# Optimization experiments

Hardware: AMD Instinct MI355X
Metric: run time of the kernel (lower is better)

Reference implementation:

```python
import jax, jax.numpy as jnp
import numpy as np

N = 50000
E = 1600000
NFEAT = 256
NHID = 256
PAD_N = 60000


def setup_inputs() -> dict:
    key = jax.random.key(0)
    ks = jax.random.split(key, 8)
    x = jax.random.normal(ks[0], (N, NFEAT), dtype=jnp.float32)
    adj_rows = jax.random.randint(ks[1], (E,), 0, N)
    adj_cols = jax.random.randint(ks[2], (E,), 0, N)
    adj_vals = jax.random.uniform(ks[3], (E,), dtype=jnp.float32)
    pos_idx = jnp.arange(N)  # unique rows within padded output
    W1 = jax.random.normal(ks[4], (NFEAT, NHID), dtype=jnp.float32) * 0.05
    b1 = jax.random.normal(ks[5], (NHID,), dtype=jnp.float32) * 0.05
    W2 = jax.random.normal(ks[6], (NHID, NHID), dtype=jnp.float32) * 0.05
    b2 = jax.random.normal(ks[7], (NHID,), dtype=jnp.float32) * 0.05
    return {"x": x, "adj_rows": adj_rows, "adj_cols": adj_cols,
            "adj_vals": adj_vals, "pad_n": PAD_N, "pos_idx": pos_idx,
            "W1": W1, "b1": b1, "W2": W2, "b2": b2}


def _graph_conv(x, rows, cols, vals, W, b):
    # support = x @ W ; out = adj @ support + b  (adj in COO form)
    support = x @ W                                   # [N, H]
    msgs = vals[:, None] * support[cols]              # [E, H] gather + scale
    agg = jax.ops.segment_sum(msgs, rows, num_segments=x.shape[0])
    return agg + b


def reference(x, adj_rows, adj_cols, adj_vals, pad_n, pos_idx, W1, b1, W2, b2):
    h = jax.nn.relu(_graph_conv(x, adj_rows, adj_cols, adj_vals, W1, b1))
    # dropout: eval mode (training=False) -> identity
    h = jax.nn.relu(_graph_conv(h, adj_rows, adj_cols, adj_vals, W2, b2))
    out = jnp.zeros((pad_n, h.shape[1]), dtype=h.dtype)
    out = out.at[pos_idx].set(h)
    return out
```

## Files before the change

kernel.cpp:

```cpp
#include <hip/hip_runtime.h>
#include <hip/hip_bf16.h>

typedef __attribute__((ext_vector_type(8))) short short8;
typedef __attribute__((ext_vector_type(4))) float f32x4;
typedef __attribute__((ext_vector_type(2))) float f32x2;

#define BUK_SHIFT 7
#define BUK_ROWS 128
#define MAXBUK 400
#define CAP2 6144
#define CHUNK 6250
#define CHUNK_PAD 6272

static __device__ __forceinline__ unsigned short f2bf(float f) {
    unsigned u = __float_as_uint(f);
    u += 0x7fffu + ((u >> 16) & 1u);
    return (unsigned short)(u >> 16);
}
static __device__ __forceinline__ unsigned pk2bf(float a, float b) {
    return (unsigned)f2bf(a) | ((unsigned)f2bf(b) << 16);
}

__global__ void wtr_kernel(const float* __restrict__ W1, const float* __restrict__ W2,
                           unsigned short* __restrict__ W1t, unsigned short* __restrict__ W2t) {
    int k = blockIdx.x, n = threadIdx.x;
    const float* W = blockIdx.y ? W2 : W1;
    unsigned short* Wt = blockIdx.y ? W2t : W1t;
    Wt[n * 256 + k] = f2bf(W[k * 256 + n]);
}


__global__ __launch_bounds__(1024) void bin_count(const int* __restrict__ rows,
                                                  int* __restrict__ cntM, int E, int nbuk) {
    __shared__ int c[MAXBUK];
    for (int i = threadIdx.x; i < nbuk; i += 1024) c[i] = 0;
    __syncthreads();
    int s = blockIdx.x * CHUNK, e = s + CHUNK < E ? s + CHUNK : E;
    for (int i = s + (int)threadIdx.x; i < e; i += 1024) atomicAdd(&c[rows[i] >> BUK_SHIFT], 1);
    __syncthreads();
    for (int i = threadIdx.x; i < nbuk; i += 1024) cntM[i * gridDim.x + blockIdx.x] = c[i];
}

__global__ __launch_bounds__(1024) void scan1_kernel(const int* __restrict__ in,
                                                     int* __restrict__ tmp,
                                                     int* __restrict__ bsum, int n) {
    __shared__ int sdata[1024];
    int i = blockIdx.x * 1024 + threadIdx.x;
    int v = (i < n) ? in[i] : 0;
    sdata[threadIdx.x] = v;
    __syncthreads();
    for (int off = 1; off < 1024; off <<= 1) {
        int t = (threadIdx.x >= (unsigned)off) ? sdata[threadIdx.x - off] : 0;
        __syncthreads();
        sdata[threadIdx.x] += t;
        __syncthreads();
    }
    if (i < n) tmp[i] = sdata[threadIdx.x] - v;
    if (threadIdx.x == 1023) bsum[blockIdx.x] = sdata[1023];
}

__global__ __launch_bounds__(512) void scan2_kernel(const int* __restrict__ bsum,
                                                    int* __restrict__ boff, int nb) {
    __shared__ int s[512];
    int t = threadIdx.x;
    int v = (t < nb) ? bsum[t] : 0;
    s[t] = v;
    __syncthreads();
    for (int off = 1; off < 512; off <<= 1) {
        int x = (t >= off) ? s[t - off] : 0;
        __syncthreads();
        s[t] += x;
        __syncthreads();
    }
    if (t < nb) boff[t] = s[t] - v;
}

static __device__ __forceinline__ int scanv(const int* __restrict__ tmp,
                                            const int* __restrict__ boff, int idx) {
    return tmp[idx] + boff[idx >> 10];
}

__global__ __launch_bounds__(1024) void bin_scatter(const int* __restrict__ rows,
                                                    const int* __restrict__ cols,
                                                    const float* __restrict__ vals,
                                                    const int* __restrict__ tmp,
                                                    const int* __restrict__ boff,
                                                    unsigned int* __restrict__ cc,
                                                    unsigned char* __restrict__ rb,
                                                    int E, int nbuk, int nblk) {
    __shared__ unsigned int scc[CHUNK_PAD];
    __shared__ unsigned char srb[CHUNK_PAD];
    __shared__ int lcnt[512], lsc[512], lcur[512];
    const int b = blockIdx.x, tid = threadIdx.x;
    const int s = b * CHUNK, e = s + CHUNK < E ? s + CHUNK : E;
    if (tid < 512) lcnt[tid] = 0;
    __syncthreads();
    for (int i = s + tid; i < e; i += 1024) atomicAdd(&lcnt[rows[i] >> BUK_SHIFT], 1);
    __syncthreads();
    if (tid < 512) lsc[tid] = lcnt[tid];
    __syncthreads();
    for (int off = 1; off < 512; off <<= 1) {
        int t = (tid < 512 && tid >= off) ? lsc[tid - off] : 0;
        __syncthreads();
        if (tid < 512) lsc[tid] += t;
        __syncthreads();
    }
    if (tid < 512) lcur[tid] = lsc[tid] - lcnt[tid];
    __syncthreads();
    for (int i = s + tid; i < e; i += 1024) {
        int r = rows[i];
        int p = atomicAdd(&lcur[r >> BUK_SHIFT], 1);
        scc[p] = ((unsigned)cols[i] << 16) | (unsigned)f2bf(vals[i]);
        srb[p] = (unsigned char)(r & (BUK_ROWS - 1));
    }
    __syncthreads();
    const int wv = tid >> 6, ln = tid & 63;
    for (int bu = wv; bu < nbuk; bu += 16) {
        const int lo = lsc[bu] - lcnt[bu];
        const int n = lcnt[bu];
        const int gbase = scanv(tmp, boff, bu * nblk + b);
        for (int j = ln; j < n; j += 64) {
            cc[gbase + j] = scc[lo + j];
            rb[gbase + j] = srb[lo + j];
        }
    }
}

__global__ __launch_bounds__(1024) void bucket_pad(const unsigned int* __restrict__ cc,
                                                   const unsigned char* __restrict__ rb,
                                                   const int* __restrict__ tmp,
                                                   const int* __restrict__ boff,
                                                   unsigned int* __restrict__ cc2,
                                                   int2* __restrict__ rp,
                                                   int E, int nbuk, int nblk, int N) {
    __shared__ int cnt[BUK_ROWS];
    __shared__ int psc[BUK_ROWS];
    __shared__ int cur[BUK_ROWS];
    const int b = blockIdx.x;
    const int tid = threadIdx.x;
    const int base = scanv(tmp, boff, b * nblk);
    const int end = (b + 1 < nbuk) ? scanv(tmp, boff, (b + 1) * nblk) : E;
    const int sz = end - base;
    if (tid < BUK_ROWS) cnt[tid] = 0;
    __syncthreads();
    for (int i = tid; i < sz; i += 1024) atomicAdd(&cnt[rb[base + i]], 1);
    __syncthreads();
    if (tid < BUK_ROWS) psc[tid] = (cnt[tid] + 7) & ~7;
    __syncthreads();
    for (int off = 1; off < BUK_ROWS; off <<= 1) {
        int t = (tid < BUK_ROWS && tid >= off) ? psc[tid - off] : 0;
        __syncthreads();
        if (tid < BUK_ROWS) psc[tid] += t;
        __syncthreads();
    }
    if (tid < BUK_ROWS) {
        int c = cnt[tid];
        int pc = (c + 7) & ~7;
        int excl = psc[tid] - pc;
        cur[tid] = excl;
        int st = b * CAP2 + excl;
        rp[b * BUK_ROWS + tid] = make_int2(st, st + pc);
        for (int z = c; z < pc; ++z) cc2[(size_t)st + z] = 0u;
    }
    __syncthreads();
    for (int i = tid; i < sz; i += 1024) {
        int p = atomicAdd(&cur[rb[base + i]], 1);
        cc2[(size_t)b * CAP2 + p] = cc[base + i];
    }
}

template <int AF32>
static __device__ __forceinline__ uint4 load_frag(const char* p) {
    if (AF32) {
        const float* f = (const float*)p;
        float4 f0 = *reinterpret_cast<const float4*>(f);
        float4 f1 = *reinterpret_cast<const float4*>(f + 4);
        uint4 u;
        u.x = pk2bf(f0.x, f0.y); u.y = pk2bf(f0.z, f0.w);
        u.z = pk2bf(f1.x, f1.y); u.w = pk2bf(f1.z, f1.w);
        return u;
    }
    return *reinterpret_cast<const uint4*>(p);
}

template <int AF32>
__global__ __launch_bounds__(256) void gemm_kernel(const void* __restrict__ Av,
                                                   const unsigned short* __restrict__ Bt,
                                                   unsigned char* __restrict__ S8, int M) {
    __shared__ unsigned char lds[2][8192];
    const int esz = AF32 ? 4 : 2;
    const int tid = threadIdx.x;
    const int lane = tid & 63;
    const int wave = tid >> 6;
    const int m0 = blockIdx.x * 64;
    const int l15 = lane & 15;
    const int q = lane >> 4;
    const int sw = (l15 & 7) << 4;

    const int st_r0 = tid >> 3;
    const int st_c = tid & 7;
    const int st_off0 = st_r0 * 128 + ((st_c ^ (st_r0 & 7)) << 4);
    const int st_r1 = st_r0 + 32;
    const int st_off1 = st_r1 * 128 + ((st_c ^ (st_r1 & 7)) << 4);
    int row0 = m0 + st_r0; row0 = row0 < M ? row0 : 0;
    int row1 = m0 + st_r1; row1 = row1 < M ? row1 : 0;
    const char* s0p = (const char*)Av + ((size_t)row0 * 256 + st_c * 8) * esz;
    const char* s1p = (const char*)Av + ((size_t)row1 * 256 + st_c * 8) * esz;

    const unsigned short* bb = Bt + (size_t)(wave * 64 + l15) * 256 + q * 8;

    f32x4 acc[4][4] = {};

    uint4 s0 = load_frag<AF32>(s0p);
    uint4 s1 = load_frag<AF32>(s1p);
    *reinterpret_cast<uint4*>(&lds[0][st_off0]) = s0;
    *reinterpret_cast<uint4*>(&lds[0][st_off1]) = s1;
    __syncthreads();

#pragma unroll
    for (int it = 0; it < 4; ++it) {
        const int buf = it & 1;
        if (it < 3) {
            s0 = load_frag<AF32>(s0p + (size_t)(it + 1) * 64 * esz);
            s1 = load_frag<AF32>(s1p + (size_t)(it + 1) * 64 * esz);
        }
        const int kk = it * 64;
#pragma unroll
        for (int ks = 0; ks < 2; ++ks) {
            short8 a[4], b[4];
#pragma unroll
            for (int mf = 0; mf < 4; ++mf) {
                int r = mf * 16 + l15;
                a[mf] = *reinterpret_cast<const short8*>(
                    &lds[buf][r * 128 + ((ks * 64 + q * 16) ^ sw)]);
            }
#pragma unroll
            for (int nf = 0; nf < 4; ++nf)
                b[nf] = *reinterpret_cast<const short8*>(bb + (size_t)nf * 16 * 256 + kk + ks * 32);
#pragma unroll
            for (int mf = 0; mf < 4; ++mf)
#pragma unroll
                for (int nf = 0; nf < 4; ++nf)
                    acc[mf][nf] = __builtin_amdgcn_mfma_f32_16x16x32_bf16(b[nf], a[mf], acc[mf][nf], 0, 0, 0);
        }
        if (it < 3) {
            *reinterpret_cast<uint4*>(&lds[buf ^ 1][st_off0]) = s0;
            *reinterpret_cast<uint4*>(&lds[buf ^ 1][st_off1]) = s1;
        }
        __syncthreads();
    }

    const int g4 = q * 4;
#pragma unroll
    for (int mf = 0; mf < 4; ++mf) {
        int m = m0 + mf * 16 + l15;
        if (m < M) {
#pragma unroll
            for (int nf = 0; nf < 4; ++nf) {
                int p = __builtin_amdgcn_cvt_pk_fp8_f32(acc[mf][nf][0], acc[mf][nf][1], 0, false);
                p = __builtin_amdgcn_cvt_pk_fp8_f32(acc[mf][nf][2], acc[mf][nf][3], p, true);
                *reinterpret_cast<int*>(S8 + ((size_t)wave * M + m) * 64 + nf * 16 + g4) = p;
            }
        }
    }
}

template <int LAYER2>
__global__ __launch_bounds__(256) void spmm_kernel(const unsigned char* __restrict__ S8,
                                                   const int2* __restrict__ rp,
                                                   const unsigned int* __restrict__ cc,
                                                   const float* __restrict__ bias,
                                                   unsigned short* __restrict__ out_bf,
                                                   float* __restrict__ out_f,
                                                   const int* __restrict__ pos_idx, int N) {
    const int sp = blockIdx.y;
    const int lane = threadIdx.x & 63;
    const int wid = threadIdx.x >> 6;
    const int q = lane >> 4;
    const int l = lane & 15;
    const int row = blockIdx.x * 16 + wid * 4 + q;
    const int2 r = rp[row];
    const unsigned lbyte = (unsigned)l * 4;
    const unsigned char* __restrict__ SA = S8 + (size_t)(2 * sp) * N * 64;
    const unsigned char* __restrict__ SB = SA + (size_t)N * 64;
    f32x2 aA01 = {0.f, 0.f}, aA23 = {0.f, 0.f}, aB01 = {0.f, 0.f}, aB23 = {0.f, 0.f};
    int i = r.x;
    if (i < r.y) {
        uint4 c0 = *reinterpret_cast<const uint4*>(cc + i);
        uint4 c1 = *reinterpret_cast<const uint4*>(cc + i + 4);
        for (; i < r.y; i += 8) {
            uint4 n0 = *reinterpret_cast<const uint4*>(cc + i + 8);
            uint4 n1 = *reinterpret_cast<const uint4*>(cc + i + 12);
            unsigned cw[8] = {c0.x, c0.y, c0.z, c0.w, c1.x, c1.y, c1.z, c1.w};
            unsigned wA[8], wB[8];
#pragma unroll
            for (int e = 0; e < 8; ++e) {
                unsigned off = ((cw[e] >> 16) << 6) + lbyte;
                wA[e] = *reinterpret_cast<const unsigned*>(SA + off);
                wB[e] = *reinterpret_cast<const unsigned*>(SB + off);
            }
#pragma unroll
            for (int e = 0; e < 8; ++e) {
                float v = __uint_as_float(cw[e] << 16);
                f32x2 vv = {v, v};
                aA01 += vv * __builtin_amdgcn_cvt_pk_f32_fp8((int)wA[e], false);
                aA23 += vv * __builtin_amdgcn_cvt_pk_f32_fp8((int)wA[e], true);
                aB01 += vv * __builtin_amdgcn_cvt_pk_f32_fp8((int)wB[e], false);
                aB23 += vv * __builtin_amdgcn_cvt_pk_f32_fp8((int)wB[e], true);
            }
            c0 = n0; c1 = n1;
        }
    }
    if (row >= N) return;
    const int fA = sp * 128 + l * 4;
    const int fB = fA + 64;
    float a0 = fmaxf(aA01.x + bias[fA + 0], 0.f);
    float a1 = fmaxf(aA01.y + bias[fA + 1], 0.f);
    float a2 = fmaxf(aA23.x + bias[fA + 2], 0.f);
    float a3 = fmaxf(aA23.y + bias[fA + 3], 0.f);
    float b0 = fmaxf(aB01.x + bias[fB + 0], 0.f);
    float b1 = fmaxf(aB01.y + bias[fB + 1], 0.f);
    float b2 = fmaxf(aB23.x + bias[fB + 2], 0.f);
    float b3 = fmaxf(aB23.y + bias[fB + 3], 0.f);
    if (LAYER2) {
        int orow = pos_idx[row];
        float* o = out_f + (size_t)orow * 256;
        *reinterpret_cast<float4*>(o + fA) = make_float4(a0, a1, a2, a3);
        *reinterpret_cast<float4*>(o + fB) = make_float4(b0, b1, b2, b3);
    } else {
        ushort4 oa, ob;
        oa.x = f2bf(a0); oa.y = f2bf(a1); oa.z = f2bf(a2); oa.w = f2bf(a3);
        ob.x = f2bf(b0); ob.y = f2bf(b1); ob.z = f2bf(b2); ob.w = f2bf(b3);
        unsigned short* o = out_bf + (size_t)row * 256;
        *reinterpret_cast<ushort4*>(o + fA) = oa;
        *reinterpret_cast<ushort4*>(o + fB) = ob;
    }
}

extern "C" void kernel_launch(void* const* d_in, const int* in_sizes, int n_in,
                              void* d_out, int out_size, void* d_ws, size_t ws_size,
                              hipStream_t stream) {
    const float* x        = (const float*)d_in[0];
    const int* adj_rows   = (const int*)d_in[1];
    const int* adj_cols   = (const int*)d_in[2];
    const float* adj_vals = (const float*)d_in[3];
    const int* pos_idx    = (const int*)d_in[5];
    const float* W1       = (const float*)d_in[6];
    const float* b1       = (const float*)d_in[7];
    const float* W2       = (const float*)d_in[8];
    const float* b2       = (const float*)d_in[9];

    const int N = in_sizes[0] / 256;
    const int E = in_sizes[1];
    const int nbuk = (N + BUK_ROWS - 1) >> BUK_SHIFT;
    const int nblk = (E + CHUNK - 1) / CHUNK;
    const int n2 = nbuk * nblk;
    const int nb2 = (n2 + 1023) / 1024;
    const int nwork = nbuk * BUK_ROWS;

    char* ws = (char*)d_ws;
    size_t off = 0;
    auto alloc = [&](size_t bytes) {
        char* p = ws + off;
        off += (bytes + 255) & ~(size_t)255;
        return p;
    };
    unsigned short* xb   = (unsigned short*)alloc((size_t)N * 256 * 2);
    unsigned char*  sup8 = (unsigned char*)alloc((size_t)N * 256);
    unsigned short* w1t  = (unsigned short*)alloc(256 * 256 * 2);
    unsigned short* w2t  = (unsigned short*)alloc(256 * 256 * 2);
    int2* rp     = (int2*)alloc((size_t)nwork * 8);
    int* cntM    = (int*)alloc((size_t)n2 * 4);
    int* tmp     = (int*)alloc((size_t)n2 * 4);
    int* bsum    = (int*)alloc(512 * 4);
    int* boff    = (int*)alloc(512 * 4);
    unsigned int* cc  = (unsigned int*)alloc((size_t)E * 4);
    unsigned char* rb = (unsigned char*)alloc((size_t)E);
    unsigned int* cc2 = (unsigned int*)alloc((size_t)nbuk * CAP2 * 4);
    (void)ws_size; (void)n_in;

    hipMemsetAsync((float*)d_out + (size_t)N * 256, 0,
                   ((size_t)out_size - (size_t)N * 256) * 4, stream);

    wtr_kernel<<<dim3(256, 2), 256, 0, stream>>>(W1, W2, w1t, w2t);

    bin_count<<<nblk, 1024, 0, stream>>>(adj_rows, cntM, E, nbuk);
    scan1_kernel<<<nb2, 1024, 0, stream>>>(cntM, tmp, bsum, n2);
    scan2_kernel<<<1, 512, 0, stream>>>(bsum, boff, nb2);
    bin_scatter<<<nblk, 1024, 0, stream>>>(adj_rows, adj_cols, adj_vals, tmp, boff, cc, rb, E, nbuk, nblk);
    bucket_pad<<<nbuk, 1024, 0, stream>>>(cc, rb, tmp, boff, cc2, rp, E, nbuk, nblk, N);

    const int ggrid = (N + 63) / 64;
    const dim3 sgrid(nwork / 16, 2);
    gemm_kernel<1><<<ggrid, 256, 0, stream>>>(x, w1t, sup8, N);
    spmm_kernel<0><<<sgrid, 256, 0, stream>>>(sup8, rp, cc2, b1, xb, nullptr, nullptr, N);
    gemm_kernel<0><<<ggrid, 256, 0, stream>>>(xb, w2t, sup8, N);
    spmm_kernel<1><<<sgrid, 256, 0, stream>>>(sup8, rp, cc2, b2, nullptr, (float*)d_out, pos_idx, N);
}
```

Before: 245.6 us.

## Remap SpMM threads to 4 lanes per row with 16-byte gathers

The SpMM kernel now assigns 4 lanes per row, each gathering a 16-byte (16 fp8 feature) chunk of one 64-feature slab, instead of 16 lanes per row each loading two 4-byte words. The grid becomes 4 feature slabs by rows/64, so each wave covers 16 rows. The aim is fewer, wider gather instructions per edge and more rows in flight per wave. The cost is more accumulators per thread, possible divergence across rows of differing lengths within a wave, and four re-reads of the column index stream instead of two.

```diff
diff --git a/kernel.cpp b/kernel.cpp
--- a/kernel.cpp
+++ b/kernel.cpp
@@ -273,67 +273,65 @@
                                                    unsigned short* __restrict__ out_bf,
                                                    float* __restrict__ out_f,
                                                    const int* __restrict__ pos_idx, int N) {
-    const int sp = blockIdx.y;
+    const int slab = blockIdx.y;
     const int lane = threadIdx.x & 63;
     const int wid = threadIdx.x >> 6;
-    const int q = lane >> 4;
-    const int l = lane & 15;
-    const int row = blockIdx.x * 16 + wid * 4 + q;
+    const int g = lane >> 2;
+    const int l = lane & 3;
+    const int row = blockIdx.x * 64 + wid * 16 + g;
     const int2 r = rp[row];
-    const unsigned lbyte = (unsigned)l * 4;
-    const unsigned char* __restrict__ SA = S8 + (size_t)(2 * sp) * N * 64;
-    const unsigned char* __restrict__ SB = SA + (size_t)N * 64;
-    f32x2 aA01 = {0.f, 0.f}, aA23 = {0.f, 0.f}, aB01 = {0.f, 0.f}, aB23 = {0.f, 0.f};
+    const unsigned char* __restrict__ Sl = S8 + (size_t)slab * N * 64 + l * 16;
+    f32x2 a[8] = {{0.f, 0.f}, {0.f, 0.f}, {0.f, 0.f}, {0.f, 0.f},
+                  {0.f, 0.f}, {0.f, 0.f}, {0.f, 0.f}, {0.f, 0.f}};
     int i = r.x;
     if (i < r.y) {
-        uint4 c0 = *reinterpret_cast<const uint4*>(cc + i);
-        uint4 c1 = *reinterpret_cast<const uint4*>(cc + i + 4);
-        for (; i < r.y; i += 8) {
-            uint4 n0 = *reinterpret_cast<const uint4*>(cc + i + 8);
-            uint4 n1 = *reinterpret_cast<const uint4*>(cc + i + 12);
-            unsigned cw[8] = {c0.x, c0.y, c0.z, c0.w, c1.x, c1.y, c1.z, c1.w};
-            unsigned wA[8], wB[8];
-#pragma unroll
-            for (int e = 0; e < 8; ++e) {
-                unsigned off = ((cw[e] >> 16) << 6) + lbyte;
-                wA[e] = *reinterpret_cast<const unsigned*>(SA + off);
-                wB[e] = *reinterpret_cast<const unsigned*>(SB + off);
-            }
-#pragma unroll
-            for (int e = 0; e < 8; ++e) {
-                float v = __uint_as_float(cw[e] << 16);
-                f32x2 vv = {v, v};
-                aA01 += vv * __builtin_amdgcn_cvt_pk_f32_fp8((int)wA[e], false);
-                aA23 += vv * __builtin_amdgcn_cvt_pk_f32_fp8((int)wA[e], true);
-                aB01 += vv * __builtin_amdgcn_cvt_pk_f32_fp8((int)wB[e], false);
-                aB23 += vv * __builtin_amdgcn_cvt_pk_f32_fp8((int)wB[e], true);
-            }
-            c0 = n0; c1 = n1;
+        uint4 c = *reinterpret_cast<const uint4*>(cc + i);
+        for (; i < r.y; i += 4) {
+            uint4 nx = *reinterpret_cast<const uint4*>(cc + i + 4);
+            unsigned cw0 = c.x, cw1 = c.y, cw2 = c.z, cw3 = c.w;
+            uint4 w0 = *reinterpret_cast<const uint4*>(Sl + ((size_t)(cw0 >> 16) << 6));
+            uint4 w1 = *reinterpret_cast<const uint4*>(Sl + ((size_t)(cw1 >> 16) << 6));
+            uint4 w2 = *reinterpret_cast<const uint4*>(Sl + ((size_t)(cw2 >> 16) << 6));
+            uint4 w3 = *reinterpret_cast<const uint4*>(Sl + ((size_t)(cw3 >> 16) << 6));
+#define ACC(ww, cw) { \
+            float v = __uint_as_float((cw) << 16); \
+            f32x2 vv = {v, v}; \
+            a[0] += vv * __builtin_amdgcn_cvt_pk_f32_fp8((int)ww.x, false); \
+            a[1] += vv * __builtin_amdgcn_cvt_pk_f32_fp8((int)ww.x, true);  \
+            a[2] += vv * __builtin_amdgcn_cvt_pk_f32_fp8((int)ww.y, false); \
+            a[3] += vv * __builtin_amdgcn_cvt_pk_f32_fp8((int)ww.y, true);  \
+            a[4] += vv * __builtin_amdgcn_cvt_pk_f32_fp8((int)ww.z, false); \
+            a[5] += vv * __builtin_amdgcn_cvt_pk_f32_fp8((int)ww.z, true);  \
+            a[6] += vv * __builtin_amdgcn_cvt_pk_f32_fp8((int)ww.w, false); \
+            a[7] += vv * __builtin_amdgcn_cvt_pk_f32_fp8((int)ww.w, true); }
+            ACC(w0, cw0) ACC(w1, cw1) ACC(w2, cw2) ACC(w3, cw3)
+#undef ACC
+            c = nx;
         }
     }
     if (row >= N) return;
-    const int fA = sp * 128 + l * 4;
-    const int fB = fA + 64;
-    float a0 = fmaxf(aA01.x + bias[fA + 0], 0.f);
-    float a1 = fmaxf(aA01.y + bias[fA + 1], 0.f);
-    float a2 = fmaxf(aA23.x + bias[fA + 2], 0.f);
-    float a3 = fmaxf(aA23.y + bias[fA + 3], 0.f);
-    float b0 = fmaxf(aB01.x + bias[fB + 0], 0.f);
-    float b1 = fmaxf(aB01.y + bias[fB + 1], 0.f);
-    float b2 = fmaxf(aB23.x + bias[fB + 2], 0.f);
-    float b3 = fmaxf(aB23.y + bias[fB + 3], 0.f);
+    const int f = slab * 64 + l * 16;
+    float o[16];
+#pragma unroll
+    for (int j = 0; j < 8; ++j) {
+        o[2 * j]     = fmaxf(a[j].x + bias[f + 2 * j], 0.f);
+        o[2 * j + 1] = fmaxf(a[j].y + bias[f + 2 * j + 1], 0.f);
+    }
     if (LAYER2) {
-        int orow = pos_idx[row];
-        float* o = out_f + (size_t)orow * 256;
-        *reinterpret_cast<float4*>(o + fA) = make_float4(a0, a1, a2, a3);
-        *reinterpret_cast<float4*>(o + fB) = make_float4(b0, b1, b2, b3);
+        float* op = out_f + (size_t)pos_idx[row] * 256 + f;
+#pragma unroll
+        for (int j = 0; j < 4; ++j)
+            *reinterpret_cast<float4*>(op + 4 * j) =
+                make_float4(o[4 * j], o[4 * j + 1], o[4 * j + 2], o[4 * j + 3]);
     } else {
-        ushort4 oa, ob;
-        oa.x = f2bf(a0); oa.y = f2bf(a1); oa.z = f2bf(a2); oa.w = f2bf(a3);
-        ob.x = f2bf(b0); ob.y = f2bf(b1); ob.z = f2bf(b2); ob.w = f2bf(b3);
-        unsigned short* o = out_bf + (size_t)row * 256;
-        *reinterpret_cast<ushort4*>(o + fA) = oa;
-        *reinterpret_cast<ushort4*>(o + fB) = ob;
+        unsigned short* op = out_bf + (size_t)row * 256 + f;
+#pragma unroll
+        for (int j = 0; j < 4; ++j) {
+            ushort4 u;
+            u.x = f2bf(o[4 * j]);     u.y = f2bf(o[4 * j + 1]);
+            u.z = f2bf(o[4 * j + 2]); u.w = f2bf(o[4 * j + 3]);
+            *reinterpret_cast<ushort4*>(op + 4 * j) = u;
+        }
     }
 }
 
@@ -391,7 +389,7 @@
     bucket_pad<<<nbuk, 1024, 0, stream>>>(cc, rb, tmp, boff, cc2, rp, E, nbuk, nblk, N);
 
     const int ggrid = (N + 63) / 64;
-    const dim3 sgrid(nwork / 16, 2);
+    const dim3 sgrid(nwork / 64, 4);
     gemm_kernel<1><<<ggrid, 256, 0, stream>>>(x, w1t, sup8, N);
     spmm_kernel<0><<<sgrid, 256, 0, stream>>>(sup8, rp, cc2, b1, xb, nullptr, nullptr, N);
     gemm_kernel<0><<<ggrid, 256, 0, stream>>>(xb, w2t, sup8, N);
```

New measurement: 298.2 us. +21.4%, slower.
